# Kernel tuning notes

Measured on AMD Instinct MI355X. Metric: run time of the kernel, lower is better.

The kernel has to match this reference:

```python
import jax, jax.numpy as jnp
import numpy as np

MAX_TAG = 16          # tag ids live in [0, MAX_TAG]; 0 = background
NUM_SEG = MAX_TAG + 1
LGG_VALUE = 3.0


def setup_inputs() -> dict:
    key = jax.random.key(0)
    k1, k2, k3 = jax.random.split(key, 3)
    B, C, H, W = 16, 8, 512, 512
    gt_kernel_key = jax.random.randint(k1, (B, H, W), 0, MAX_TAG + 1, dtype=jnp.int32)
    training_mask = jax.random.randint(k2, (B, H, W), 0, 2, dtype=jnp.int32)
    similarity_vector = jax.random.normal(k3, (B, C, H, W), dtype=jnp.float32)
    return {
        "gt_kernel_key": gt_kernel_key,
        "training_mask": training_mask,
        "similarity_vector": similarity_vector,
    }


def _per_sample_loss(sim_hwc, gk, mask):
    # sim_hwc: [H, W, C]; gk, mask: [H, W]
    C = sim_hwc.shape[-1]
    flat_sim = sim_hwc.reshape(-1, C)            # [HW, C]
    flat_gk = gk.reshape(-1)                     # [HW]
    ones = jnp.ones_like(flat_gk, dtype=jnp.float32)

    # segment mean per tag over the UNMASKED kernel map (matches original:
    # tags are selected with the mask, but means use gt_kernel directly)
    sums = jax.ops.segment_sum(flat_sim, flat_gk, num_segments=NUM_SEG)      # [T, C]
    counts = jax.ops.segment_sum(ones, flat_gk, num_segments=NUM_SEG)       # [T]
    means = sums / jnp.maximum(counts, 1.0)[:, None]

    # a tag participates iff it appears in gt_kernel_key * training_mask and != 0
    masked_gk = flat_gk * mask.reshape(-1)
    masked_counts = jax.ops.segment_sum(ones, masked_gk, num_segments=NUM_SEG)
    present = (masked_counts > 0).at[0].set(False)                           # [T]

    # pairwise distances between tag means (tiny: NUM_SEG x NUM_SEG)
    diff = means[:, None, :] - means[None, :, :]                             # [T, T, C]
    dist = jnp.sqrt(jnp.sum(diff * diff, axis=-1) + 1e-12)                   # [T, T]
    pair_loss = jnp.log(jnp.maximum(LGG_VALUE - dist, 0.0) ** 2 + 1.0)

    valid = present[:, None] & present[None, :] & ~jnp.eye(NUM_SEG, dtype=bool)
    n_valid = jnp.sum(valid.astype(jnp.float32))
    loss = jnp.sum(jnp.where(valid, pair_loss, 0.0)) / jnp.maximum(n_valid, 1.0)
    sample_valid = (jnp.sum(present.astype(jnp.int32)) >= 2).astype(jnp.float32)
    return loss, sample_valid


def reference(gt_kernel_key, training_mask, similarity_vector):
    # [B, C, H, W] -> [B, H, W, C]
    sim = jnp.transpose(similarity_vector, (0, 2, 3, 1))
    losses, valids = jax.vmap(_per_sample_loss)(sim, gt_kernel_key, training_mask)
    n = jnp.sum(valids)
    return jnp.where(n > 0, jnp.sum(losses * valids) / jnp.maximum(n, 1.0), 0.0)
```

## Files before the change

### kernel.cpp

```cpp
#include <hip/hip_runtime.h>

#define NB 16
#define NC 8
#define HW (512*512)
#define NT 16
#define LGG 3.0f

#define BLOCKS 2048
#define THREADS 256
#define BPSAMP (BLOCKS/NB)
#define PXB (HW/BPSAMP)
#define TILE 512
#define NTILES (PXB/TILE)
#define JITERS (TILE/128)
#define NCHUNK (2 + 2*NC)
#define NCOL 10
#define ACCW (NT*NCOL)

#define SIM_LDS 2048
#define PLANE_STRIDE 2064
#define LDS_BYTES (SIM_LDS + NC*PLANE_STRIDE)

typedef __attribute__((ext_vector_type(8))) short bf16x8;
typedef __attribute__((ext_vector_type(4))) float f32x4;

__device__ __forceinline__ unsigned pk_bf16(float x, float y) {
    unsigned r;
    asm("v_cvt_pk_bf16_f32 %0, %1, %2" : "=v"(r) : "v"(x), "v"(y));
    return r;
}

__device__ __forceinline__ unsigned onehot2(int a, int b, int r1) {
    return (a == r1 ? 0x3F80u : 0u) | (b == r1 ? 0x3F800000u : 0u);
}
__device__ __forceinline__ unsigned mask2(int a, int b) {
    return (a ? 0x3F80u : 0u) | (b ? 0x3F800000u : 0u);
}

__device__ __forceinline__ void gload_lds16(const void* g, void* lds) {
    __builtin_amdgcn_global_load_lds(
        (const __attribute__((address_space(1))) void*)g,
        (__attribute__((address_space(3))) void*)lds, 16, 0, 0);
}

__global__ __launch_bounds__(256) void init_ws(float* g_acc) {
    const int i = threadIdx.x;
    #pragma unroll
    for (int k = 0; k < NB*ACCW; k += 256)
        if (k + i < NB*ACCW) g_acc[k + i] = 0.f;
}

__global__ __launch_bounds__(THREADS) void accum(
    const int* __restrict__ gk, const int* __restrict__ mask,
    const float* __restrict__ sim, float* __restrict__ g_acc)
{
    const int tid  = threadIdx.x;
    const int lane = tid & 63, wid = tid >> 6;
    const int bid  = blockIdx.x;
    const int b    = bid / BPSAMP;
    const int sb   = bid % BPSAMP;
    const int c    = lane & 15;
    const int l4   = lane >> 4;
    const int base = sb * PXB;

    __shared__ __align__(16) char ldsbuf[LDS_BYTES];

    const int*   gkS = gk   + (size_t)b * HW + base;
    const int*   mkS = mask + (size_t)b * HW + base;
    const float* smS = sim  + (size_t)b * NC * HW + base;

    f32x4 acc = {0.f, 0.f, 0.f, 0.f};
    const int r1 = c + 1;
    const int simoff = SIM_LDS + (c & 7) * PLANE_STRIDE;

    for (int t = 0; t < NTILES; ++t) {
        const int t0 = t * TILE;
        #pragma unroll
        for (int k = 0; k < 5; ++k) {
            const int idx = wid + 4 * k;
            if (idx < NCHUNK) {
                const void* src;
                int dst;
                if (idx < 2) {
                    src = gkS + t0 + idx * 256 + lane * 4;
                    dst = idx * 1024;
                } else {
                    const int p = (idx - 2) >> 1, h = (idx - 2) & 1;
                    src = smS + (size_t)p * HW + t0 + h * 256 + lane * 4;
                    dst = SIM_LDS + p * PLANE_STRIDE + h * 1024;
                }
                gload_lds16(src, ldsbuf + dst);
            }
        }
        int4 mc0, mc1;
        if (c == 9) {
            const int* mp = mkS + t0 + wid * 128 + l4 * 8;
            mc0 = *(const int4*)mp; mc1 = *(const int4*)(mp + 4);
        }
        __syncthreads();

        #pragma unroll
        for (int j = 0; j < JITERS; ++j) {
            int4 mn0, mn1;
            if (j + 1 < JITERS && c == 9) {
                const int* mp = mkS + t0 + wid * 128 + (j + 1) * 32 + l4 * 8;
                mn0 = *(const int4*)mp; mn1 = *(const int4*)(mp + 4);
            }
            const int px = wid * 128 + j * 32 + l4 * 8;
            const int4 g0 = *(const int4*)(ldsbuf + px * 4);
            const int4 g1 = *(const int4*)(ldsbuf + px * 4 + 16);
            const float4 v0 = *(const float4*)(ldsbuf + simoff + px * 4);
            const float4 v1 = *(const float4*)(ldsbuf + simoff + px * 4 + 16);

            union { bf16x8 v; unsigned u[4]; } A, B;
            A.u[0] = onehot2(g0.x, g0.y, r1);
            A.u[1] = onehot2(g0.z, g0.w, r1);
            A.u[2] = onehot2(g1.x, g1.y, r1);
            A.u[3] = onehot2(g1.z, g1.w, r1);
            const unsigned bs0 = pk_bf16(v0.x, v0.y), bs1 = pk_bf16(v0.z, v0.w);
            const unsigned bs2 = pk_bf16(v1.x, v1.y), bs3 = pk_bf16(v1.z, v1.w);
            const unsigned bm0 = mask2(mc0.x, mc0.y), bm1 = mask2(mc0.z, mc0.w);
            const unsigned bm2 = mask2(mc1.x, mc1.y), bm3 = mask2(mc1.z, mc1.w);
            B.u[0] = c < 8 ? bs0 : (c == 8 ? 0x3F803F80u : (c == 9 ? bm0 : 0u));
            B.u[1] = c < 8 ? bs1 : (c == 8 ? 0x3F803F80u : (c == 9 ? bm1 : 0u));
            B.u[2] = c < 8 ? bs2 : (c == 8 ? 0x3F803F80u : (c == 9 ? bm2 : 0u));
            B.u[3] = c < 8 ? bs3 : (c == 8 ? 0x3F803F80u : (c == 9 ? bm3 : 0u));

            acc = __builtin_amdgcn_mfma_f32_16x16x32_bf16(A.v, B.v, acc, 0, 0, 0);
            mc0 = mn0; mc1 = mn1;
        }
        __syncthreads();
    }

    float* lred = (float*)ldsbuf;
    const int row0 = l4 * 4;
    #pragma unroll
    for (int i = 0; i < 4; ++i) lred[wid * 256 + (row0 + i) * 16 + c] = acc[i];
    __syncthreads();

    if (tid < NT * NCOL) {
        const int r = tid / NCOL, cc = tid % NCOL;
        const float s = lred[0*256 + r*16 + cc] + lred[1*256 + r*16 + cc]
                      + lred[2*256 + r*16 + cc] + lred[3*256 + r*16 + cc];
        atomicAdd(&g_acc[b * ACCW + tid], s);
    }
}

__global__ __launch_bounds__(256) void finalize(
    const float* __restrict__ g_acc, float* __restrict__ out)
{
    __shared__ float    means[NB][NT][NC];
    __shared__ unsigned pres[NB];
    __shared__ float    sl[NB], sn[NB];
    const int tid = threadIdx.x;

    if (tid < NB) pres[tid] = 0u;
    __syncthreads();

    {
        const int b = tid >> 4, t = tid & 15;
        const float* row = g_acc + b * ACCW + t * NCOL;
        const float cnt = row[8];
        const float mc  = row[9];
        const float inv = 1.f / fmaxf(cnt, 1.f);
        #pragma unroll
        for (int cc = 0; cc < NC; ++cc) means[b][t][cc] = row[cc] * inv;
        if (mc > 0.5f) atomicOr(&pres[b], 1u << (t + 1));
    }
    __syncthreads();

    const int b = tid >> 4, i = tid & 15;
    const unsigned pr = pres[b];
    float loss = 0.f, nv = 0.f;
    if ((pr >> (i + 1)) & 1u) {
        #pragma unroll
        for (int j = 0; j < NT; ++j) {
            if (j != i && ((pr >> (j + 1)) & 1u)) {
                float d2 = 0.f;
                #pragma unroll
                for (int cc = 0; cc < NC; ++cc) {
                    const float d = means[b][i][cc] - means[b][j][cc];
                    d2 += d * d;
                }
                const float dist = sqrtf(d2 + 1e-12f);
                const float r = fmaxf(LGG - dist, 0.f);
                loss += logf(r * r + 1.f);
                nv += 1.f;
            }
        }
    }
    #pragma unroll
    for (int o = 8; o; o >>= 1) { loss += __shfl_xor(loss, o); nv += __shfl_xor(nv, o); }
    if (i == 0) {
        const float v = (__popc(pr) >= 2) ? 1.f : 0.f;
        sl[b] = v * (loss / fmaxf(nv, 1.f));
        sn[b] = v;
    }
    __syncthreads();
    if (tid == 0) {
        float tl = 0.f, tv = 0.f;
        for (int bb = 0; bb < NB; ++bb) { tl += sl[bb]; tv += sn[bb]; }
        out[0] = (tv > 0.f) ? tl / tv : 0.f;
    }
}

extern "C" void kernel_launch(void* const* d_in, const int* in_sizes, int n_in,
                              void* d_out, int out_size, void* d_ws, size_t ws_size,
                              hipStream_t stream) {
    const int*   gk   = (const int*)d_in[0];
    const int*   mask = (const int*)d_in[1];
    const float* sim  = (const float*)d_in[2];
    float* out   = (float*)d_out;
    float* g_acc = (float*)d_ws;

    init_ws<<<1, 256, 0, stream>>>(g_acc);
    accum<<<BLOCKS, THREADS, 0, stream>>>(gk, mask, sim, g_acc);
    finalize<<<1, 256, 0, stream>>>(g_acc, out);
}
```

Measured before the change: 44.99 us.

## Double-buffer LDS tiles with async prefetch and stage mask via LDS

Adds a two-buffer LDS pipeline: the next tile's gk, mask and sim chunks are issued via global_load_lds while the current tile is consumed, with a partial vmcnt wait instead of a full sync. The mask now goes through LDS instead of per-lane global loads. The sim planes use a rotated placement in place of padding to avoid bank conflicts. Halving the block count gives each block more tiles to pipeline, at the cost of fewer blocks for latency hiding and tricky raw waitcnt/barrier ordering.

```diff
diff --git a/kernel.cpp b/kernel.cpp
--- a/kernel.cpp
+++ b/kernel.cpp
@@ -6,20 +6,21 @@
 #define NT 16
 #define LGG 3.0f
 
-#define BLOCKS 2048
+#define BLOCKS 1024
 #define THREADS 256
 #define BPSAMP (BLOCKS/NB)
 #define PXB (HW/BPSAMP)
 #define TILE 512
 #define NTILES (PXB/TILE)
-#define JITERS (TILE/128)
-#define NCHUNK (2 + 2*NC)
+#define JITERS 4
 #define NCOL 10
 #define ACCW (NT*NCOL)
 
-#define SIM_LDS 2048
-#define PLANE_STRIDE 2064
-#define LDS_BYTES (SIM_LDS + NC*PLANE_STRIDE)
+#define GK_OFF  0
+#define MK_OFF  2048
+#define SIM_OFF 4096
+#define BUF_BYTES 20480
+#define LDS_BYTES (2*BUF_BYTES)
 
 typedef __attribute__((ext_vector_type(8))) short bf16x8;
 typedef __attribute__((ext_vector_type(4))) float f32x4;
@@ -29,18 +30,40 @@
     asm("v_cvt_pk_bf16_f32 %0, %1, %2" : "=v"(r) : "v"(x), "v"(y));
     return r;
 }
-
 __device__ __forceinline__ unsigned onehot2(int a, int b, int r1) {
     return (a == r1 ? 0x3F80u : 0u) | (b == r1 ? 0x3F800000u : 0u);
 }
 __device__ __forceinline__ unsigned mask2(int a, int b) {
     return (a ? 0x3F80u : 0u) | (b ? 0x3F800000u : 0u);
 }
-
 __device__ __forceinline__ void gload_lds16(const void* g, void* lds) {
     __builtin_amdgcn_global_load_lds(
         (const __attribute__((address_space(1))) void*)g,
         (__attribute__((address_space(3))) void*)lds, 16, 0, 0);
+}
+
+__device__ __forceinline__ void stage(const char* gkB, const char* mkB,
+                                      const char* smB, char* buf,
+                                      int t0b, int wid, int lane) {
+    #pragma unroll
+    for (int k = 0; k < 5; ++k) {
+        const int idx = wid + 4 * k;
+        const char* src; int dst;
+        if (idx < 2) {
+            src = gkB + t0b + idx * 1024 + lane * 16;
+            dst = GK_OFF + idx * 1024 + lane * 16;
+        } else if (idx < 4) {
+            src = mkB + t0b + (idx - 2) * 1024 + lane * 16;
+            dst = MK_OFF + (idx - 2) * 1024 + lane * 16;
+        } else {
+            const int s = idx - 4, p = s >> 1, h = s & 1;
+            const int local = h * 1024 + lane * 16;
+            const int goff = (local - 16 * p) & 2047;
+            src = smB + (size_t)p * (HW * 4) + t0b + goff;
+            dst = SIM_OFF + p * 2048 + local;
+        }
+        gload_lds16(src, buf + dst);
+    }
 }
 
 __global__ __launch_bounds__(256) void init_ws(float* g_acc) {
@@ -63,54 +86,48 @@
     const int l4   = lane >> 4;
     const int base = sb * PXB;
 
-    __shared__ __align__(16) char ldsbuf[LDS_BYTES];
-
-    const int*   gkS = gk   + (size_t)b * HW + base;
-    const int*   mkS = mask + (size_t)b * HW + base;
-    const float* smS = sim  + (size_t)b * NC * HW + base;
+    __shared__ __align__(16) char lds[LDS_BYTES];
+
+    const char* gkB = (const char*)(gk   + (size_t)b * HW + base);
+    const char* mkB = (const char*)(mask + (size_t)b * HW + base);
+    const char* smB = (const char*)(sim  + (size_t)b * NC * HW + base);
 
     f32x4 acc = {0.f, 0.f, 0.f, 0.f};
     const int r1 = c + 1;
-    const int simoff = SIM_LDS + (c & 7) * PLANE_STRIDE;
-
+    const int pl = c & 7;
+    const int rot = 16 * pl;
+
+    stage(gkB, mkB, smB, lds, 0, wid, lane);
+
+    #pragma unroll 1
     for (int t = 0; t < NTILES; ++t) {
-        const int t0 = t * TILE;
-        #pragma unroll
-        for (int k = 0; k < 5; ++k) {
-            const int idx = wid + 4 * k;
-            if (idx < NCHUNK) {
-                const void* src;
-                int dst;
-                if (idx < 2) {
-                    src = gkS + t0 + idx * 256 + lane * 4;
-                    dst = idx * 1024;
-                } else {
-                    const int p = (idx - 2) >> 1, h = (idx - 2) & 1;
-                    src = smS + (size_t)p * HW + t0 + h * 256 + lane * 4;
-                    dst = SIM_LDS + p * PLANE_STRIDE + h * 1024;
-                }
-                gload_lds16(src, ldsbuf + dst);
-            }
-        }
-        int4 mc0, mc1;
-        if (c == 9) {
-            const int* mp = mkS + t0 + wid * 128 + l4 * 8;
-            mc0 = *(const int4*)mp; mc1 = *(const int4*)(mp + 4);
-        }
-        __syncthreads();
+        char* cur = lds + (t & 1) * BUF_BYTES;
+        if (t + 1 < NTILES) {
+            stage(gkB, mkB, smB, lds + ((t + 1) & 1) * BUF_BYTES,
+                  (t + 1) * (TILE * 4), wid, lane);
+            asm volatile("s_waitcnt vmcnt(5)" ::: "memory");
+        } else {
+            asm volatile("s_waitcnt vmcnt(0)" ::: "memory");
+        }
+        __builtin_amdgcn_sched_barrier(0);
+        __builtin_amdgcn_s_barrier();
 
         #pragma unroll
         for (int j = 0; j < JITERS; ++j) {
-            int4 mn0, mn1;
-            if (j + 1 < JITERS && c == 9) {
-                const int* mp = mkS + t0 + wid * 128 + (j + 1) * 32 + l4 * 8;
-                mn0 = *(const int4*)mp; mn1 = *(const int4*)(mp + 4);
+            const int o = (wid * 128 + j * 32 + l4 * 8) * 4;
+            const int4 g0 = *(const int4*)(cur + GK_OFF + o);
+            const int4 g1 = *(const int4*)(cur + GK_OFF + o + 16);
+            float4 v0 = {0,0,0,0}, v1 = {0,0,0,0};
+            if (c < 8) {
+                const char* sp = cur + SIM_OFF + pl * 2048;
+                v0 = *(const float4*)(sp + ((o + rot) & 2047));
+                v1 = *(const float4*)(sp + ((o + 16 + rot) & 2047));
             }
-            const int px = wid * 128 + j * 32 + l4 * 8;
-            const int4 g0 = *(const int4*)(ldsbuf + px * 4);
-            const int4 g1 = *(const int4*)(ldsbuf + px * 4 + 16);
-            const float4 v0 = *(const float4*)(ldsbuf + simoff + px * 4);
-            const float4 v1 = *(const float4*)(ldsbuf + simoff + px * 4 + 16);
+            int4 m0 = {0,0,0,0}, m1 = {0,0,0,0};
+            if (c == 9) {
+                m0 = *(const int4*)(cur + MK_OFF + o);
+                m1 = *(const int4*)(cur + MK_OFF + o + 16);
+            }
 
             union { bf16x8 v; unsigned u[4]; } A, B;
             A.u[0] = onehot2(g0.x, g0.y, r1);
@@ -119,20 +136,19 @@
             A.u[3] = onehot2(g1.z, g1.w, r1);
             const unsigned bs0 = pk_bf16(v0.x, v0.y), bs1 = pk_bf16(v0.z, v0.w);
             const unsigned bs2 = pk_bf16(v1.x, v1.y), bs3 = pk_bf16(v1.z, v1.w);
-            const unsigned bm0 = mask2(mc0.x, mc0.y), bm1 = mask2(mc0.z, mc0.w);
-            const unsigned bm2 = mask2(mc1.x, mc1.y), bm3 = mask2(mc1.z, mc1.w);
+            const unsigned bm0 = mask2(m0.x, m0.y), bm1 = mask2(m0.z, m0.w);
+            const unsigned bm2 = mask2(m1.x, m1.y), bm3 = mask2(m1.z, m1.w);
             B.u[0] = c < 8 ? bs0 : (c == 8 ? 0x3F803F80u : (c == 9 ? bm0 : 0u));
             B.u[1] = c < 8 ? bs1 : (c == 8 ? 0x3F803F80u : (c == 9 ? bm1 : 0u));
             B.u[2] = c < 8 ? bs2 : (c == 8 ? 0x3F803F80u : (c == 9 ? bm2 : 0u));
             B.u[3] = c < 8 ? bs3 : (c == 8 ? 0x3F803F80u : (c == 9 ? bm3 : 0u));
 
             acc = __builtin_amdgcn_mfma_f32_16x16x32_bf16(A.v, B.v, acc, 0, 0, 0);
-            mc0 = mn0; mc1 = mn1;
-        }
-        __syncthreads();
-    }
-
-    float* lred = (float*)ldsbuf;
+        }
+        __builtin_amdgcn_s_barrier();
+    }
+
+    float* lred = (float*)lds;
     const int row0 = l4 * 4;
     #pragma unroll
     for (int i = 0; i < 4; ++i) lred[wid * 256 + (row0 + i) * 16 + c] = acc[i];
```

Measured after the change: 44.70 us. About the same (-0.6%).
